# Optimization experiments

Hardware: AMD Instinct MI355X
Metric: run time of the kernel (lower is better)

## Reference

```python
import jax, jax.numpy as jnp
import numpy as np

B, S = 512, 512
VOCAB, E, H1, H2, NTAGS = 50000, 20, 30, 50, 45


def _xavier_scale(fan_in, fan_out):
    return float(np.sqrt(2.0 / (fan_in + fan_out)))


def setup_inputs() -> dict:
    key = jax.random.key(0)
    ks = jax.random.split(key, 32)
    n = lambda i, shape, s=1.0: jax.random.normal(ks[i], shape, dtype=jnp.float32) * s
    w = 0.1  # weight scale
    emb_f1 = n(0, (VOCAB, E), w).at[0].set(0.0)  # padding_idx=0
    emb_b1 = n(1, (VOCAB, E), w).at[0].set(0.0)
    xs1 = _xavier_scale(B, H1)
    xs2 = _xavier_scale(B, H2)
    inp = {
        "x": jax.random.randint(ks[2], (B, S), 0, VOCAB, dtype=jnp.int64),
        "emb_f1": emb_f1, "emb_b1": emb_b1,
        "h0_f1": n(3, (B, H1), xs1), "c0_f1": n(4, (B, H1), xs1),
        "Wih_f1": n(5, (4 * H1, E), w), "Whh_f1": n(6, (4 * H1, H1), w),
        "bih_f1": n(7, (4 * H1,), w), "bhh_f1": n(8, (4 * H1,), w),
        "h0_b1": n(9, (B, H1), xs1), "c0_b1": n(10, (B, H1), xs1),
        "Wih_b1": n(11, (4 * H1, E), w), "Whh_b1": n(12, (4 * H1, H1), w),
        "bih_b1": n(13, (4 * H1,), w), "bhh_b1": n(14, (4 * H1,), w),
        "h0_f2": n(15, (B, H2), xs2), "c0_f2": n(16, (B, H2), xs2),
        "Wih_f2": n(17, (4 * H2, 2 * H1), w), "Whh_f2": n(18, (4 * H2, H2), w),
        "bih_f2": n(19, (4 * H2,), w), "bhh_f2": n(20, (4 * H2,), w),
        "h0_b2": n(21, (B, H2), xs2), "c0_b2": n(22, (B, H2), xs2),
        "Wih_b2": n(23, (4 * H2, 2 * H1), w), "Whh_b2": n(24, (4 * H2, H2), w),
        "bih_b2": n(25, (4 * H2,), w), "bhh_b2": n(26, (4 * H2,), w),
        "lin_w": n(27, (NTAGS, 2 * H2), w), "lin_b": n(28, (NTAGS,), w),
    }
    return inp


def _run_lstm(seq, h0, c0, Wih, Whh, bih, bhh, forward):
    """PyTorch LSTMCell recurrence over seq (B,S,D). Replicates the original's
    quirks: backward dir appends hidden states in reversed time order, and the
    (S,B,H) stack is .view()-ed into (B,S,H) without transposing."""
    b, s, _ = seq.shape
    h = h0.shape[-1]
    xs = jnp.swapaxes(seq, 0, 1)  # (S,B,D)

    def step(carry, xt):
        hh, cc = carry
        g = xt @ Wih.T + bih + hh @ Whh.T + bhh  # (B, 4H), gate order i,f,g,o
        i, f, gg, o = jnp.split(g, 4, axis=-1)
        cc = jax.nn.sigmoid(f) * cc + jax.nn.sigmoid(i) * jnp.tanh(gg)
        hh = jax.nn.sigmoid(o) * jnp.tanh(cc)
        return (hh, cc), hh

    _, hs = jax.lax.scan(step, (h0, c0), xs, reverse=not forward)  # hs[i] ~ time i
    if not forward:
        hs = hs[::-1]  # torch appended in processing (reversed-time) order
    return hs.reshape(b, s, h)  # faithful buggy view (S,B,H) -> (B,S,H)


def reference(x, emb_f1, emb_b1,
              h0_f1, c0_f1, Wih_f1, Whh_f1, bih_f1, bhh_f1,
              h0_b1, c0_b1, Wih_b1, Whh_b1, bih_b1, bhh_b1,
              h0_f2, c0_f2, Wih_f2, Whh_f2, bih_f2, bhh_f2,
              h0_b2, c0_b2, Wih_b2, Whh_b2, bih_b2, bhh_b2,
              lin_w, lin_b):
    f1 = _run_lstm(emb_f1[x], h0_f1, c0_f1, Wih_f1, Whh_f1, bih_f1, bhh_f1, True)
    b1 = _run_lstm(emb_b1[x], h0_b1, c0_b1, Wih_b1, Whh_b1, bih_b1, bhh_b1, False)
    l1 = jnp.concatenate([f1, b1], axis=2)  # (B,S,2*H1)
    f2 = _run_lstm(l1, h0_f2, c0_f2, Wih_f2, Whh_f2, bih_f2, bhh_f2, True)
    b2 = _run_lstm(l1, h0_b2, c0_b2, Wih_b2, Whh_b2, bih_b2, bhh_b2, False)
    l2 = jnp.concatenate([f2, b2], axis=2)  # (B,S,2*H2)
    return l2 @ lin_w.T + lin_b  # (B,S,NTAGS)
```

## Files before the change

### kernel.cpp

```cpp
#include <hip/hip_runtime.h>
#include <hip/hip_bf16.h>

typedef __hip_bfloat16 bf16;
typedef __attribute__((ext_vector_type(8))) short short8;
typedef __attribute__((ext_vector_type(4))) float float4v;
typedef unsigned short ushort_t;

#define BB 512
#define SS 512
#define EE 20
#define H1C 30
#define H2C 50
#define NTC 45

#define BAR() asm volatile("s_waitcnt lgkmcnt(0)\n\ts_barrier" ::: "memory")

#if __has_builtin(__builtin_amdgcn_exp2f)
#define EXP2(x) __builtin_amdgcn_exp2f(x)
#else
#define EXP2(x) exp2f(x)
#endif
#if __has_builtin(__builtin_amdgcn_rcpf)
#define RCPF(x) __builtin_amdgcn_rcpf(x)
#else
#define RCPF(x) (1.0f / (x))
#endif

__device__ __forceinline__ float sigf(float v) {
    return RCPF(1.0f + EXP2(-1.4426950408889634f * v));
}
__device__ __forceinline__ float tanh_(float v) {
    return 2.0f * RCPF(1.0f + EXP2(-2.8853900817779268f * v)) - 1.0f;
}

__device__ __forceinline__ ushort_t f2bf(float f) {
    unsigned u = __float_as_uint(f);
    unsigned r = u + 0x7FFFu + ((u >> 16) & 1u);
    return (ushort_t)(r >> 16);
}
__device__ __forceinline__ float bf2f(ushort_t s) { return __uint_as_float(((unsigned)s) << 16); }

__device__ __forceinline__ float ldG(const void* p, int i, int f32) {
    if (f32) return ((const float*)p)[i];
    return bf2f(((const ushort_t*)p)[i]);
}
__device__ __forceinline__ int ldTok(const void* x, int i, int x64) {
    const int* xi = (const int*)x;
    return x64 ? xi[2 * i] : xi[i];
}

__global__ void detect_kernel(const void* bih, const void* x, int* flags) {
    if (threadIdx.x == 0 && blockIdx.x == 0) {
        const ushort_t* u = (const ushort_t*)bih;
        int isf = 0;
        for (int i = 0; i < 120; i++) {
            float v = fabsf(bf2f(u[i]));
            if (!(v < 16.0f)) isf = 1;
        }
        flags[0] = isf;
        const int* xi = (const int*)x;
        int orv = 0;
        for (int i = 1; i < 32; i += 2) orv |= xi[i];
        flags[1] = (orv == 0) ? 1 : 0;
    }
}

struct XV4 { float v[4]; };

__global__ __launch_bounds__(128) void lstm1_kernel(
    const void* __restrict__ x,
    const void* __restrict__ emb_f, const void* __restrict__ emb_b,
    const void* __restrict__ h0_f, const void* __restrict__ c0_f,
    const void* __restrict__ Wih_f, const void* __restrict__ Whh_f,
    const void* __restrict__ bih_f, const void* __restrict__ bhh_f,
    const void* __restrict__ h0_b, const void* __restrict__ c0_b,
    const void* __restrict__ Wih_b, const void* __restrict__ Whh_b,
    const void* __restrict__ bih_b, const void* __restrict__ bhh_b,
    ushort_t* __restrict__ hsf, ushort_t* __restrict__ hsb,
    const int* __restrict__ flags)
{
    const int f32v = flags[0], x64 = flags[1];
    const int wg = blockIdx.x, dir = wg >> 5, j0 = (wg & 31) << 4, tid = threadIdx.x;
    const int wave = tid >> 6, lane = tid & 63, li = lane & 15, quad = lane >> 4;

    const void* emb = dir ? emb_b : emb_f;
    const void* h0  = dir ? h0_b  : h0_f;
    const void* c0  = dir ? c0_b  : c0_f;
    const void* Wih = dir ? Wih_b : Wih_f;
    const void* Whh = dir ? Whh_b : Whh_f;
    const void* bih = dir ? bih_b : bih_f;
    const void* bhh = dir ? bhh_b : bhh_f;
    ushort_t* hs = dir ? hsb : hsf;

    __shared__ __align__(16) ushort_t Af[2][2][64][8];
    __shared__ int toks[16][SS];

    for (int idx = tid; idx < 16 * SS; idx += 128) {
        int r = idx >> 9, t = idx & (SS - 1);
        toks[r][t] = ldTok(x, (j0 + r) * SS + t, x64);
    }
    for (int idx = tid; idx < 2 * 2 * 64 * 8; idx += 128) ((ushort_t*)Af)[idx] = 0;

    const int n = wave * 16 + li;
    const bool nok = n < H1C;

    short8 bhi[4][2], blo[4][2];
    float bias_g[4];
    #pragma unroll
    for (int g = 0; g < 4; g++) {
        const int wrow = g * H1C + n;
        bias_g[g] = nok ? (ldG(bih, wrow, f32v) + ldG(bhh, wrow, f32v)) : 0.f;
        #pragma unroll
        for (int kt = 0; kt < 2; kt++) {
            short8 hi, lo;
            #pragma unroll
            for (int j = 0; j < 8; j++) {
                int k = kt * 32 + quad * 8 + j;
                float w = 0.f;
                if (nok) {
                    if (k < EE) w = ldG(Wih, wrow * EE + k, f32v);
                    else if (k < EE + H1C) w = ldG(Whh, wrow * H1C + (k - EE), f32v);
                }
                ushort_t h = f2bf(w);
                hi[j] = (short)h;
                lo[j] = (short)f2bf(w - bf2f(h));
            }
            bhi[g][kt] = hi; blo[g][kt] = lo;
        }
    }

    const int kh = EE + n;
    const int khk = kh >> 5, khg = (kh & 31) >> 3, khj = kh & 7;
    const int lrow = tid / 5, lc = tid - lrow * 5, k0 = lc * 4;
    const bool ldr = tid < 80;
    const int t0 = dir ? SS - 1 : 0, dt = dir ? -1 : 1;

    __syncthreads();

    float creg[4];
    #pragma unroll
    for (int r = 0; r < 4; r++) {
        const int m = quad * 4 + r;
        creg[r] = nok ? ldG(c0, (j0 + m) * H1C + n, f32v) : 0.f;
        ushort_t hb = nok ? f2bf(ldG(h0, (j0 + m) * H1C + n, f32v)) : 0;
        Af[0][khk][khg * 16 + m][khj] = hb;
    }
    XV4 xA, xB;
    if (ldr) {
        int tok = toks[lrow][t0];
        #pragma unroll
        for (int jj = 0; jj < 4; jj++)
            Af[0][0][(k0 >> 3) * 16 + lrow][(k0 & 7) + jj] = f2bf(ldG(emb, tok * EE + k0 + jj, f32v));
        int tok1 = toks[lrow][t0 + dt];
        #pragma unroll
        for (int jj = 0; jj < 4; jj++) xA.v[jj] = ldG(emb, tok1 * EE + k0 + jj, f32v);
    }
    __syncthreads();

    auto step = [&](int it, XV4& xin, XV4& xout) {
        const int t = t0 + dt * it;
        const int cur = it & 1, nxt = cur ^ 1;
        BAR();
        short8 af0 = *(const short8*)&Af[cur][0][lane][0];
        short8 af1 = *(const short8*)&Af[cur][1][lane][0];
        if (ldr && it + 2 < SS) {
            int tok = toks[lrow][t + 2 * dt];
            #pragma unroll
            for (int jj = 0; jj < 4; jj++) xout.v[jj] = ldG(emb, tok * EE + k0 + jj, f32v);
        }
        float4v acc[4];
        #pragma unroll
        for (int g = 0; g < 4; g++) {
            float4v a; a[0] = a[1] = a[2] = a[3] = bias_g[g];
            a = __builtin_amdgcn_mfma_f32_16x16x32_bf16(af0, bhi[g][0], a, 0, 0, 0);
            a = __builtin_amdgcn_mfma_f32_16x16x32_bf16(af0, blo[g][0], a, 0, 0, 0);
            a = __builtin_amdgcn_mfma_f32_16x16x32_bf16(af1, bhi[g][1], a, 0, 0, 0);
            a = __builtin_amdgcn_mfma_f32_16x16x32_bf16(af1, blo[g][1], a, 0, 0, 0);
            acc[g] = a;
        }
        ushort_t hb[4];
        #pragma unroll
        for (int r = 0; r < 4; r++) {
            float gi = acc[0][r], gf = acc[1][r], gg = acc[2][r], go = acc[3][r];
            float c = sigf(gf) * creg[r] + sigf(gi) * tanh_(gg);
            float h = sigf(go) * tanh_(c);
            creg[r] = c;
            hb[r] = nok ? f2bf(h) : 0;
            hs[((size_t)(j0 + quad * 4 + r) * SS + t) * 32 + n] = hb[r];
        }
        if (it + 1 < SS) {
            #pragma unroll
            for (int r = 0; r < 4; r++) Af[nxt][khk][khg * 16 + quad * 4 + r][khj] = hb[r];
            if (ldr) {
                #pragma unroll
                for (int jj = 0; jj < 4; jj++)
                    Af[nxt][0][(k0 >> 3) * 16 + lrow][(k0 & 7) + jj] = f2bf(xin.v[jj]);
            }
        }
    };
    for (int it = 0; it < SS; it += 2) { step(it, xA, xB); step(it + 1, xB, xA); }
}

__global__ __launch_bounds__(256) void lstm2_kernel(
    const ushort_t* __restrict__ hs1f, const ushort_t* __restrict__ hs1b,
    const void* __restrict__ h0_f, const void* __restrict__ c0_f,
    const void* __restrict__ Wih_f, const void* __restrict__ Whh_f,
    const void* __restrict__ bih_f, const void* __restrict__ bhh_f,
    const void* __restrict__ h0_b, const void* __restrict__ c0_b,
    const void* __restrict__ Wih_b, const void* __restrict__ Whh_b,
    const void* __restrict__ bih_b, const void* __restrict__ bhh_b,
    ushort_t* __restrict__ hsf, ushort_t* __restrict__ hsb,
    const int* __restrict__ flags)
{
    const int f32v = flags[0];
    const int wg = blockIdx.x, dir = wg >> 5, cb = (wg & 31) << 4, tid = threadIdx.x;
    const int wave = tid >> 6, lane = tid & 63, li = lane & 15, quad = lane >> 4;

    const void* h0  = dir ? h0_b  : h0_f;
    const void* c0  = dir ? c0_b  : c0_f;
    const void* Wih = dir ? Wih_b : Wih_f;
    const void* Whh = dir ? Whh_b : Whh_f;
    const void* bih = dir ? bih_b : bih_f;
    const void* bhh = dir ? bhh_b : bhh_f;
    ushort_t* hs = dir ? hsb : hsf;

    __shared__ __align__(16) ushort_t Af[2][4][64][8];
    for (int idx = tid; idx < 2 * 4 * 64 * 8; idx += 256) ((ushort_t*)Af)[idx] = 0;

    const int n = wave * 16 + li;
    const bool nok = n < H2C;

    short8 bhi[4][4], blo[4][4];
    float bias_g[4];
    #pragma unroll
    for (int g = 0; g < 4; g++) {
        const int wrow = g * H2C + n;
        bias_g[g] = nok ? (ldG(bih, wrow, f32v) + ldG(bhh, wrow, f32v)) : 0.f;
        #pragma unroll
        for (int kt = 0; kt < 4; kt++) {
            short8 hi, lo;
            #pragma unroll
            for (int j = 0; j < 8; j++) {
                int k = kt * 32 + quad * 8 + j;
                float w = 0.f;
                if (nok) {
                    if (k < H1C) w = ldG(Wih, wrow * (2 * H1C) + k, f32v);
                    else if (k >= 32 && k < 32 + H1C) w = ldG(Wih, wrow * (2 * H1C) + H1C + (k - 32), f32v);
                    else if (k >= 64 && k < 64 + H2C) w = ldG(Whh, wrow * H2C + (k - 64), f32v);
                }
                ushort_t h = f2bf(w);
                hi[j] = (short)h;
                lo[j] = (short)f2bf(w - bf2f(h));
            }
            bhi[g][kt] = hi; blo[g][kt] = lo;
        }
    }

    const int kh = 64 + n;
    const int khk = kh >> 5, khg = (kh & 31) >> 3, khj = kh & 7;
    const int lrow = tid >> 4, k0 = (tid & 15) * 4;
    const int t0 = dir ? SS - 1 : 0, dt = dir ? -1 : 1;

    auto loadX = [&](int c) -> ushort4 {
        const int a = cb + lrow;
        if (k0 < 32)
            return *(const ushort4*)&hs1f[((size_t)c * SS + a) * 32 + k0];
        else
            return *(const ushort4*)&hs1b[((size_t)c * SS + (SS - 1 - a)) * 32 + (k0 - 32)];
    };

    __syncthreads();

    float creg[4];
    #pragma unroll
    for (int r = 0; r < 4; r++) {
        const int m = quad * 4 + r;
        creg[r] = nok ? ldG(c0, (cb + m) * H2C + n, f32v) : 0.f;
        ushort_t hb = nok ? f2bf(ldG(h0, (cb + m) * H2C + n, f32v)) : 0;
        Af[0][khk][khg * 16 + m][khj] = hb;
    }
    {
        ushort4 xi = loadX(t0);
        const int kg = (k0 & 31) >> 3, kt = k0 >> 5, jb = k0 & 7;
        Af[0][kt][kg * 16 + lrow][jb + 0] = xi.x;
        Af[0][kt][kg * 16 + lrow][jb + 1] = xi.y;
        Af[0][kt][kg * 16 + lrow][jb + 2] = xi.z;
        Af[0][kt][kg * 16 + lrow][jb + 3] = xi.w;
    }
    ushort4 xA = loadX(t0 + dt), xB;
    __syncthreads();

    auto step = [&](int it, ushort4& xin, ushort4& xout) {
        const int c = t0 + dt * it;
        const int cur = it & 1, nxt = cur ^ 1;
        BAR();
        short8 af[4];
        #pragma unroll
        for (int kt = 0; kt < 4; kt++) af[kt] = *(const short8*)&Af[cur][kt][lane][0];
        if (it + 2 < SS) xout = loadX(c + 2 * dt);
        float4v acc[4];
        #pragma unroll
        for (int g = 0; g < 4; g++) {
            float4v a; a[0] = a[1] = a[2] = a[3] = bias_g[g];
            #pragma unroll
            for (int kt = 0; kt < 4; kt++) {
                a = __builtin_amdgcn_mfma_f32_16x16x32_bf16(af[kt], bhi[g][kt], a, 0, 0, 0);
                a = __builtin_amdgcn_mfma_f32_16x16x32_bf16(af[kt], blo[g][kt], a, 0, 0, 0);
            }
            acc[g] = a;
        }
        ushort_t hb[4];
        #pragma unroll
        for (int r = 0; r < 4; r++) {
            float gi = acc[0][r], gf = acc[1][r], gg = acc[2][r], go = acc[3][r];
            float cc = sigf(gf) * creg[r] + sigf(gi) * tanh_(gg);
            float h = sigf(go) * tanh_(cc);
            creg[r] = cc;
            hb[r] = nok ? f2bf(h) : 0;
        }
        ushort4 h4; h4.x = hb[0]; h4.y = hb[1]; h4.z = hb[2]; h4.w = hb[3];
        *(ushort4*)&hs[((size_t)c * 64 + n) * SS + cb + quad * 4] = h4;
        if (it + 1 < SS) {
            #pragma unroll
            for (int r = 0; r < 4; r++) Af[nxt][khk][khg * 16 + quad * 4 + r][khj] = hb[r];
            const int kg = (k0 & 31) >> 3, kt = k0 >> 5, jb = k0 & 7;
            Af[nxt][kt][kg * 16 + lrow][jb + 0] = xin.x;
            Af[nxt][kt][kg * 16 + lrow][jb + 1] = xin.y;
            Af[nxt][kt][kg * 16 + lrow][jb + 2] = xin.z;
            Af[nxt][kt][kg * 16 + lrow][jb + 3] = xin.w;
        }
    };
    for (int it = 0; it < SS; it += 2) { step(it, xA, xB); step(it + 1, xB, xA); }
}

__global__ __launch_bounds__(256) void lin_kernel(
    const ushort_t* __restrict__ hs2f, const ushort_t* __restrict__ hs2b,
    const void* __restrict__ lw, const void* __restrict__ lb,
    void* __restrict__ out, const int* __restrict__ flags)
{
    const int f32v = flags[0];
    const int tid = threadIdx.x, wave = tid >> 6, lane = tid & 63, li = lane & 15, quad = lane >> 4;

    __shared__ __align__(16) ushort_t Af[4][4][64][8];
    for (int idx = tid; idx < 4 * 4 * 64 * 8; idx += 256) ((ushort_t*)Af)[idx] = 0;

    short8 bhi[3][4], blo[3][4];
    float biasv[3];
    #pragma unroll
    for (int nt = 0; nt < 3; nt++) {
        const int nn = nt * 16 + li;
        const bool nok = nn < NTC;
        biasv[nt] = nok ? ldG(lb, nn, f32v) : 0.f;
        #pragma unroll
        for (int kt = 0; kt < 4; kt++) {
            short8 hi, lo;
            #pragma unroll
            for (int j = 0; j < 8; j++) {
                int k = kt * 32 + quad * 8 + j;
                float w = 0.f;
                if (nok) {
                    if (k < H2C) w = ldG(lw, nn * 100 + k, f32v);
                    else if (k >= 64 && k < 64 + H2C) w = ldG(lw, nn * 100 + 50 + (k - 64), f32v);
                }
                ushort_t h = f2bf(w);
                hi[j] = (short)h;
                lo[j] = (short)f2bf(w - bf2f(h));
            }
            bhi[nt][kt] = hi; blo[nt][kt] = lo;
        }
    }

    const int P0 = blockIdx.x * 64;
    const int i = P0 >> 9, j0 = P0 & 511;
    __syncthreads();
    for (int idx = tid; idx < 100 * 32; idx += 256) {
        const int kk = idx >> 5, pj = (idx & 31) * 2;
        unsigned v;
        int k;
        if (kk < H2C) {
            v = *(const unsigned*)&hs2f[((size_t)i * 64 + kk) * SS + j0 + pj];
            k = kk;
        } else {
            v = *(const unsigned*)&hs2b[((size_t)(SS - 1 - i) * 64 + (kk - H2C)) * SS + j0 + pj];
            k = 64 + (kk - H2C);
        }
        const int kt = k >> 5, kg = (k & 31) >> 3, j = k & 7;
        Af[pj >> 4][kt][kg * 16 + (pj & 15)][j] = (ushort_t)(v & 0xFFFF);
        Af[pj >> 4][kt][kg * 16 + ((pj + 1) & 15)][j] = (ushort_t)(v >> 16);
    }
    __syncthreads();

    short8 af[4];
    #pragma unroll
    for (int kt = 0; kt < 4; kt++) af[kt] = *(const short8*)&Af[wave][kt][lane][0];
    #pragma unroll
    for (int nt = 0; nt < 3; nt++) {
        float4v a; a[0] = a[1] = a[2] = a[3] = biasv[nt];
        #pragma unroll
        for (int kt = 0; kt < 4; kt++) {
            a = __builtin_amdgcn_mfma_f32_16x16x32_bf16(af[kt], bhi[nt][kt], a, 0, 0, 0);
            a = __builtin_amdgcn_mfma_f32_16x16x32_bf16(af[kt], blo[nt][kt], a, 0, 0, 0);
        }
        const int nn = nt * 16 + li;
        if (nn < NTC) {
            #pragma unroll
            for (int reg = 0; reg < 4; reg++) {
                const int prow = wave * 16 + quad * 4 + reg;
                const size_t op = (size_t)(P0 + prow) * NTC + nn;
                if (f32v) ((float*)out)[op] = a[reg];
                else      ((ushort_t*)out)[op] = f2bf(a[reg]);
            }
        }
    }
}

extern "C" void kernel_launch(void* const* d_in, const int* in_sizes, int n_in,
                              void* d_out, int out_size, void* d_ws, size_t ws_size,
                              hipStream_t stream)
{
    const void* x      = d_in[0];
    const void* emb_f1 = d_in[1];
    const void* emb_b1 = d_in[2];
    const void* h0_f1  = d_in[3];
    const void* c0_f1  = d_in[4];
    const void* Wih_f1 = d_in[5];
    const void* Whh_f1 = d_in[6];
    const void* bih_f1 = d_in[7];
    const void* bhh_f1 = d_in[8];
    const void* h0_b1  = d_in[9];
    const void* c0_b1  = d_in[10];
    const void* Wih_b1 = d_in[11];
    const void* Whh_b1 = d_in[12];
    const void* bih_b1 = d_in[13];
    const void* bhh_b1 = d_in[14];
    const void* h0_f2  = d_in[15];
    const void* c0_f2  = d_in[16];
    const void* Wih_f2 = d_in[17];
    const void* Whh_f2 = d_in[18];
    const void* bih_f2 = d_in[19];
    const void* bhh_f2 = d_in[20];
    const void* h0_b2  = d_in[21];
    const void* c0_b2  = d_in[22];
    const void* Wih_b2 = d_in[23];
    const void* Whh_b2 = d_in[24];
    const void* bih_b2 = d_in[25];
    const void* bhh_b2 = d_in[26];
    const void* lin_w  = d_in[27];
    const void* lin_b  = d_in[28];

    int* flags = (int*)d_ws;
    ushort_t* hs1f = (ushort_t*)((char*)d_ws + 256);
    ushort_t* hs1b = hs1f + (size_t)BB * SS * 32;
    ushort_t* hs2f = hs1b + (size_t)BB * SS * 32;
    ushort_t* hs2b = hs2f + (size_t)SS * 64 * BB;

    detect_kernel<<<1, 64, 0, stream>>>(bih_f1, x, flags);
    lstm1_kernel<<<64, 128, 0, stream>>>(x, emb_f1, emb_b1,
        h0_f1, c0_f1, Wih_f1, Whh_f1, bih_f1, bhh_f1,
        h0_b1, c0_b1, Wih_b1, Whh_b1, bih_b1, bhh_b1, hs1f, hs1b, flags);
    lstm2_kernel<<<64, 256, 0, stream>>>(hs1f, hs1b,
        h0_f2, c0_f2, Wih_f2, Whh_f2, bih_f2, bhh_f2,
        h0_b2, c0_b2, Wih_b2, Whh_b2, bih_b2, bhh_b2, hs2f, hs2b, flags);
    lin_kernel<<<(BB * SS) / 64, 256, 0, stream>>>(hs2f, hs2b, lin_w, lin_b, d_out, flags);
}
```

Before: 1.004 ms.

## Split LSTM gates across waves, precompute input projection one step ahead

Both LSTM kernels now give each wave one gate (i/f/g/o) and swap MFMA operand roles so weights are the A operand. Gate pre-activations go through a shared-memory Gs buffer, and a separate thread mapping applies the nonlinearities. The input-to-hidden product for step t+1 is issued alongside the recurrent product for step t, so only the Whh part sits on the serial dependency chain. Activations fold the log2e scaling into weights and bias, share reciprocals between paired sigmoids, and embedding loads are vectorized. The cost is two barriers per step plus the LDS round trip for gates, and lstm1 now runs 256 threads instead of 128.

Result: slower. 1.433 ms (+42.8%).

```diff
diff --git a/kernel.cpp b/kernel.cpp
--- a/kernel.cpp
+++ b/kernel.cpp
@@ -1,7 +1,6 @@
 #include <hip/hip_runtime.h>
 #include <hip/hip_bf16.h>
 
-typedef __hip_bfloat16 bf16;
 typedef __attribute__((ext_vector_type(8))) short short8;
 typedef __attribute__((ext_vector_type(4))) float float4v;
 typedef unsigned short ushort_t;
@@ -26,12 +25,7 @@
 #define RCPF(x) (1.0f / (x))
 #endif
 
-__device__ __forceinline__ float sigf(float v) {
-    return RCPF(1.0f + EXP2(-1.4426950408889634f * v));
-}
-__device__ __forceinline__ float tanh_(float v) {
-    return 2.0f * RCPF(1.0f + EXP2(-2.8853900817779268f * v)) - 1.0f;
-}
+#define LOG2E 1.4426950408889634f
 
 __device__ __forceinline__ ushort_t f2bf(float f) {
     unsigned u = __float_as_uint(f);
@@ -47,6 +41,21 @@
 __device__ __forceinline__ int ldTok(const void* x, int i, int x64) {
     const int* xi = (const int*)x;
     return x64 ? xi[2 * i] : xi[i];
+}
+
+__device__ __forceinline__ float lstm_act(float gi, float gf, float gg, float go, float& c) {
+    gi = fmaxf(gi, -30.f); gf = fmaxf(gf, -30.f);
+    gg = fmaxf(gg, -30.f); go = fmaxf(go, -30.f);
+    float di = 1.f + EXP2(-gi), df = 1.f + EXP2(-gf);
+    float dg = 1.f + EXP2(-gg), dO = 1.f + EXP2(-go);
+    float r1 = RCPF(di * df), r2 = RCPF(dg * dO);
+    float si = df * r1, sf = di * r1;
+    float tg = 2.f * (dO * r2) - 1.f;
+    float so = dg * r2;
+    float cc = sf * c + si * tg;
+    c = cc;
+    float e = EXP2(-2.8853900817779268f * cc);
+    return so * (2.f * RCPF(1.f + e) - 1.f);
 }
 
 __global__ void detect_kernel(const void* bih, const void* x, int* flags) {
@@ -65,9 +74,46 @@
     }
 }
 
-struct XV4 { float v[4]; };
-
-__global__ __launch_bounds__(128) void lstm1_kernel(
+struct XR8 { uint4 a, b; };
+
+__device__ __forceinline__ XR8 ldEmb8(const void* emb, int tok, int k0, int nelem, int f32v) {
+    XR8 o;
+    if (f32v) {
+        const float* p = (const float*)emb + (size_t)tok * EE + k0;
+        o.a = *(const uint4*)p;
+        o.b = (nelem == 8) ? *(const uint4*)(p + 4) : o.a;
+    } else {
+        const ushort_t* p = (const ushort_t*)emb + (size_t)tok * EE + k0;
+        uint2 lo = *(const uint2*)p;
+        o.a.x = lo.x; o.a.y = lo.y;
+        if (nelem == 8) { uint2 hi = *(const uint2*)(p + 4); o.a.z = hi.x; o.a.w = hi.y; }
+        else { o.a.z = 0; o.a.w = 0; }
+        o.b = o.a;
+    }
+    return o;
+}
+__device__ __forceinline__ void writeX1(ushort_t* dst, const XR8& x, int nelem, int f32v) {
+    if (f32v) {
+        if (nelem == 8) {
+            short8 s;
+            s[0] = (short)f2bf(__uint_as_float(x.a.x)); s[1] = (short)f2bf(__uint_as_float(x.a.y));
+            s[2] = (short)f2bf(__uint_as_float(x.a.z)); s[3] = (short)f2bf(__uint_as_float(x.a.w));
+            s[4] = (short)f2bf(__uint_as_float(x.b.x)); s[5] = (short)f2bf(__uint_as_float(x.b.y));
+            s[6] = (short)f2bf(__uint_as_float(x.b.z)); s[7] = (short)f2bf(__uint_as_float(x.b.w));
+            *(short8*)dst = s;
+        } else {
+            ushort4 u;
+            u.x = f2bf(__uint_as_float(x.a.x)); u.y = f2bf(__uint_as_float(x.a.y));
+            u.z = f2bf(__uint_as_float(x.a.z)); u.w = f2bf(__uint_as_float(x.a.w));
+            *(ushort4*)dst = u;
+        }
+    } else {
+        if (nelem == 8) *(uint4*)dst = x.a;
+        else { uint2 t; t.x = x.a.x; t.y = x.a.y; *(uint2*)dst = t; }
+    }
+}
+
+__global__ __launch_bounds__(256, 1) void lstm1_kernel(
     const void* __restrict__ x,
     const void* __restrict__ emb_f, const void* __restrict__ emb_b,
     const void* __restrict__ h0_f, const void* __restrict__ c0_f,
@@ -80,8 +126,9 @@
     const int* __restrict__ flags)
 {
     const int f32v = flags[0], x64 = flags[1];
-    const int wg = blockIdx.x, dir = wg >> 5, j0 = (wg & 31) << 4, tid = threadIdx.x;
-    const int wave = tid >> 6, lane = tid & 63, li = lane & 15, quad = lane >> 4;
+    const int tid = threadIdx.x;
+    const int cg = blockIdx.x, dir = cg >> 5, j0 = (cg & 31) << 4;
+    const int w = tid >> 6, lane = tid & 63, li = lane & 15, quad = lane >> 4;
 
     const void* emb = dir ? emb_b : emb_f;
     const void* h0  = dir ? h0_b  : h0_f;
@@ -92,116 +139,127 @@
     const void* bhh = dir ? bhh_b : bhh_f;
     ushort_t* hs = dir ? hsb : hsf;
 
-    __shared__ __align__(16) ushort_t Af[2][2][64][8];
     __shared__ int toks[16][SS];
-
-    for (int idx = tid; idx < 16 * SS; idx += 128) {
+    __shared__ __align__(16) ushort_t Xs[2][16][48];
+    __shared__ __align__(16) ushort_t Hs[16][48];
+    __shared__ float Gs[4][16][33];
+
+    for (int idx = tid; idx < 16 * SS; idx += 256) {
         int r = idx >> 9, t = idx & (SS - 1);
         toks[r][t] = ldTok(x, (j0 + r) * SS + t, x64);
     }
-    for (int idx = tid; idx < 2 * 2 * 64 * 8; idx += 128) ((ushort_t*)Af)[idx] = 0;
-
-    const int n = wave * 16 + li;
-    const bool nok = n < H1C;
-
-    short8 bhi[4][2], blo[4][2];
-    float bias_g[4];
+    for (int idx = tid; idx < 2 * 16 * 48; idx += 256) ((ushort_t*)Xs)[idx] = 0;
+    for (int idx = tid; idx < 16 * 48; idx += 256) ((ushort_t*)Hs)[idx] = 0;
+
+    const float sc = (w == 2) ? 2.0f * LOG2E : LOG2E;
+    short8 whh_h[2], whh_l[2], wxh_[2], wxl_[2];
+    float4v biasv[2];
     #pragma unroll
-    for (int g = 0; g < 4; g++) {
-        const int wrow = g * H1C + n;
-        bias_g[g] = nok ? (ldG(bih, wrow, f32v) + ldG(bhh, wrow, f32v)) : 0.f;
-        #pragma unroll
-        for (int kt = 0; kt < 2; kt++) {
-            short8 hi, lo;
+    for (int u = 0; u < 2; u++) {
+        const int n = u * 16 + li;
+        const bool nok = n < H1C;
+        #pragma unroll
+        for (int r = 0; r < 4; r++) {
+            int nn = u * 16 + quad * 4 + r;
+            biasv[u][r] = (nn < H1C) ? sc * (ldG(bih, w * H1C + nn, f32v) + ldG(bhh, w * H1C + nn, f32v)) : 0.f;
+        }
+        short8 hh, hl, xh, xl;
+        #pragma unroll
+        for (int j = 0; j < 8; j++) {
+            const int k = quad * 8 + j;
+            float wh = (nok && k < H1C) ? sc * ldG(Whh, (w * H1C + n) * H1C + k, f32v) : 0.f;
+            ushort_t b1 = f2bf(wh); hh[j] = (short)b1; hl[j] = (short)f2bf(wh - bf2f(b1));
+            float wx = (nok && k < EE) ? sc * ldG(Wih, (w * H1C + n) * EE + k, f32v) : 0.f;
+            ushort_t b2 = f2bf(wx); xh[j] = (short)b2; xl[j] = (short)f2bf(wx - bf2f(b2));
+        }
+        whh_h[u] = hh; whh_l[u] = hl; wxh_[u] = xh; wxl_[u] = xl;
+    }
+
+    const int am = li, anb = w * 8 + quad * 2;
+    const int lm = w * 4 + quad, lch = li;
+    const bool ldr = li < 3;
+    const int lk0 = lch * 8, lnel = (lch == 2) ? 4 : 8;
+    const int t0 = dir ? SS - 1 : 0, dt = dir ? -1 : 1;
+
+    __syncthreads();
+
+    float cr0, cr1;
+    {
+        const int n0 = anb, n1 = anb + 1;
+        cr0 = (n0 < H1C) ? ldG(c0, (j0 + am) * H1C + n0, f32v) : 0.f;
+        cr1 = (n1 < H1C) ? ldG(c0, (j0 + am) * H1C + n1, f32v) : 0.f;
+        unsigned ha = (n0 < H1C) ? f2bf(ldG(h0, (j0 + am) * H1C + n0, f32v)) : 0;
+        unsigned hb = (n1 < H1C) ? f2bf(ldG(h0, (j0 + am) * H1C + n1, f32v)) : 0;
+        *(unsigned*)&Hs[am][anb] = ha | (hb << 16);
+    }
+    XR8 embA = {}, embB = {}; int tokA = 0, tokB = 0;
+    if (ldr) {
+        XR8 e0 = ldEmb8(emb, toks[lm][t0], lk0, lnel, f32v);
+        writeX1(&Xs[0][lm][lk0], e0, lnel, f32v);
+        XR8 e1 = ldEmb8(emb, toks[lm][t0 + dt], lk0, lnel, f32v);
+        writeX1(&Xs[1][lm][lk0], e1, lnel, f32v);
+        embA = ldEmb8(emb, toks[lm][t0 + 2 * dt], lk0, lnel, f32v);
+        tokA = toks[lm][t0 + 3 * dt];
+    }
+    __syncthreads();
+
+    float4v xacc[2];
+    {
+        short8 xf = *(const short8*)&Xs[0][li][quad * 8];
+        #pragma unroll
+        for (int u = 0; u < 2; u++) {
+            float4v b = biasv[u];
+            b = __builtin_amdgcn_mfma_f32_16x16x32_bf16(wxh_[u], xf, b, 0, 0, 0);
+            b = __builtin_amdgcn_mfma_f32_16x16x32_bf16(wxl_[u], xf, b, 0, 0, 0);
+            xacc[u] = b;
+        }
+    }
+
+    auto step = [&](int it, XR8& ein, XR8& eout, int& tin, int& tout) {
+        const int t = t0 + dt * it;
+        short8 hf = *(const short8*)&Hs[li][quad * 8];
+        short8 xf = *(const short8*)&Xs[(it + 1) & 1][li][quad * 8];
+        float4v acc[2], xn[2];
+        #pragma unroll
+        for (int u = 0; u < 2; u++) {
+            float4v a = xacc[u];
+            a = __builtin_amdgcn_mfma_f32_16x16x32_bf16(whh_h[u], hf, a, 0, 0, 0);
+            a = __builtin_amdgcn_mfma_f32_16x16x32_bf16(whh_l[u], hf, a, 0, 0, 0);
+            acc[u] = a;
+            float4v b = biasv[u];
+            b = __builtin_amdgcn_mfma_f32_16x16x32_bf16(wxh_[u], xf, b, 0, 0, 0);
+            b = __builtin_amdgcn_mfma_f32_16x16x32_bf16(wxl_[u], xf, b, 0, 0, 0);
+            xn[u] = b;
+        }
+        #pragma unroll
+        for (int u = 0; u < 2; u++) {
             #pragma unroll
-            for (int j = 0; j < 8; j++) {
-                int k = kt * 32 + quad * 8 + j;
-                float w = 0.f;
-                if (nok) {
-                    if (k < EE) w = ldG(Wih, wrow * EE + k, f32v);
-                    else if (k < EE + H1C) w = ldG(Whh, wrow * H1C + (k - EE), f32v);
-                }
-                ushort_t h = f2bf(w);
-                hi[j] = (short)h;
-                lo[j] = (short)f2bf(w - bf2f(h));
-            }
-            bhi[g][kt] = hi; blo[g][kt] = lo;
-        }
-    }
-
-    const int kh = EE + n;
-    const int khk = kh >> 5, khg = (kh & 31) >> 3, khj = kh & 7;
-    const int lrow = tid / 5, lc = tid - lrow * 5, k0 = lc * 4;
-    const bool ldr = tid < 80;
-    const int t0 = dir ? SS - 1 : 0, dt = dir ? -1 : 1;
-
-    __syncthreads();
-
-    float creg[4];
-    #pragma unroll
-    for (int r = 0; r < 4; r++) {
-        const int m = quad * 4 + r;
-        creg[r] = nok ? ldG(c0, (j0 + m) * H1C + n, f32v) : 0.f;
-        ushort_t hb = nok ? f2bf(ldG(h0, (j0 + m) * H1C + n, f32v)) : 0;
-        Af[0][khk][khg * 16 + m][khj] = hb;
-    }
-    XV4 xA, xB;
-    if (ldr) {
-        int tok = toks[lrow][t0];
-        #pragma unroll
-        for (int jj = 0; jj < 4; jj++)
-            Af[0][0][(k0 >> 3) * 16 + lrow][(k0 & 7) + jj] = f2bf(ldG(emb, tok * EE + k0 + jj, f32v));
-        int tok1 = toks[lrow][t0 + dt];
-        #pragma unroll
-        for (int jj = 0; jj < 4; jj++) xA.v[jj] = ldG(emb, tok1 * EE + k0 + jj, f32v);
-    }
-    __syncthreads();
-
-    auto step = [&](int it, XV4& xin, XV4& xout) {
-        const int t = t0 + dt * it;
-        const int cur = it & 1, nxt = cur ^ 1;
+            for (int r = 0; r < 4; r++)
+                Gs[w][li][u * 16 + quad * 4 + r] = acc[u][r];
+        }
         BAR();
-        short8 af0 = *(const short8*)&Af[cur][0][lane][0];
-        short8 af1 = *(const short8*)&Af[cur][1][lane][0];
-        if (ldr && it + 2 < SS) {
-            int tok = toks[lrow][t + 2 * dt];
-            #pragma unroll
-            for (int jj = 0; jj < 4; jj++) xout.v[jj] = ldG(emb, tok * EE + k0 + jj, f32v);
-        }
-        float4v acc[4];
-        #pragma unroll
-        for (int g = 0; g < 4; g++) {
-            float4v a; a[0] = a[1] = a[2] = a[3] = bias_g[g];
-            a = __builtin_amdgcn_mfma_f32_16x16x32_bf16(af0, bhi[g][0], a, 0, 0, 0);
-            a = __builtin_amdgcn_mfma_f32_16x16x32_bf16(af0, blo[g][0], a, 0, 0, 0);
-            a = __builtin_amdgcn_mfma_f32_16x16x32_bf16(af1, bhi[g][1], a, 0, 0, 0);
-            a = __builtin_amdgcn_mfma_f32_16x16x32_bf16(af1, blo[g][1], a, 0, 0, 0);
-            acc[g] = a;
-        }
-        ushort_t hb[4];
-        #pragma unroll
-        for (int r = 0; r < 4; r++) {
-            float gi = acc[0][r], gf = acc[1][r], gg = acc[2][r], go = acc[3][r];
-            float c = sigf(gf) * creg[r] + sigf(gi) * tanh_(gg);
-            float h = sigf(go) * tanh_(c);
-            creg[r] = c;
-            hb[r] = nok ? f2bf(h) : 0;
-            hs[((size_t)(j0 + quad * 4 + r) * SS + t) * 32 + n] = hb[r];
-        }
-        if (it + 1 < SS) {
-            #pragma unroll
-            for (int r = 0; r < 4; r++) Af[nxt][khk][khg * 16 + quad * 4 + r][khj] = hb[r];
-            if (ldr) {
-                #pragma unroll
-                for (int jj = 0; jj < 4; jj++)
-                    Af[nxt][0][(k0 >> 3) * 16 + lrow][(k0 & 7) + jj] = f2bf(xin.v[jj]);
-            }
-        }
+        float gi0 = Gs[0][am][anb], gi1 = Gs[0][am][anb + 1];
+        float gf0 = Gs[1][am][anb], gf1 = Gs[1][am][anb + 1];
+        float gg0 = Gs[2][am][anb], gg1 = Gs[2][am][anb + 1];
+        float go0 = Gs[3][am][anb], go1 = Gs[3][am][anb + 1];
+        float h0v = lstm_act(gi0, gf0, gg0, go0, cr0);
+        float h1v = lstm_act(gi1, gf1, gg1, go1, cr1);
+        unsigned hp = (unsigned)f2bf(h0v) | ((unsigned)f2bf(h1v) << 16);
+        *(unsigned*)&Hs[am][anb] = hp;
+        *(unsigned*)&hs[((size_t)(j0 + am) * SS + t) * 32 + anb] = hp;
+        if (ldr) {
+            if (it + 2 < SS) writeX1(&Xs[it & 1][lm][lk0], ein, lnel, f32v);
+            if (it + 3 < SS) eout = ldEmb8(emb, tin, lk0, lnel, f32v);
+            if (it + 4 < SS) tout = toks[lm][t0 + dt * (it + 4)];
+        }
+        #pragma unroll
+        for (int u = 0; u < 2; u++) xacc[u] = xn[u];
+        BAR();
     };
-    for (int it = 0; it < SS; it += 2) { step(it, xA, xB); step(it + 1, xB, xA); }
-}
-
-__global__ __launch_bounds__(256) void lstm2_kernel(
+    for (int it = 0; it < SS; it += 2) { step(it, embA, embB, tokA, tokB); step(it + 1, embB, embA, tokB, tokA); }
+}
+
+__global__ __launch_bounds__(256, 1) void lstm2_kernel(
     const ushort_t* __restrict__ hs1f, const ushort_t* __restrict__ hs1b,
     const void* __restrict__ h0_f, const void* __restrict__ c0_f,
     const void* __restrict__ Wih_f, const void* __restrict__ Whh_f,
@@ -213,8 +271,9 @@
     const int* __restrict__ flags)
 {
     const int f32v = flags[0];
-    const int wg = blockIdx.x, dir = wg >> 5, cb = (wg & 31) << 4, tid = threadIdx.x;
-    const int wave = tid >> 6, lane = tid & 63, li = lane & 15, quad = lane >> 4;
+    const int tid = threadIdx.x;
+    const int cg = blockIdx.x, dir = cg >> 5, cb = (cg & 31) << 4;
+    const int w = tid >> 6, lane = tid & 63, li = lane & 15, quad = lane >> 4;
 
     const void* h0  = dir ? h0_b  : h0_f;
     const void* c0  = dir ? c0_b  : c0_f;
@@ -224,113 +283,138 @@
     const void* bhh = dir ? bhh_b : bhh_f;
     ushort_t* hs = dir ? hsb : hsf;
 
-    __shared__ __align__(16) ushort_t Af[2][4][64][8];
-    for (int idx = tid; idx < 2 * 4 * 64 * 8; idx += 256) ((ushort_t*)Af)[idx] = 0;
-
-    const int n = wave * 16 + li;
-    const bool nok = n < H2C;
-
-    short8 bhi[4][4], blo[4][4];
-    float bias_g[4];
+    __shared__ __align__(16) ushort_t Xs[2][16][112];
+    __shared__ __align__(16) ushort_t Hs[16][112];
+    __shared__ float Gs[4][16][65];
+
+    for (int idx = tid; idx < 2 * 16 * 112; idx += 256) ((ushort_t*)Xs)[idx] = 0;
+    for (int idx = tid; idx < 16 * 112; idx += 256) ((ushort_t*)Hs)[idx] = 0;
+
+    const float sc = (w == 2) ? 2.0f * LOG2E : LOG2E;
+    short8 wh_h[4][2], wh_l[4][2], wx_h[4][2], wx_l[4][2];
+    float4v biasv[4];
     #pragma unroll
-    for (int g = 0; g < 4; g++) {
-        const int wrow = g * H2C + n;
-        bias_g[g] = nok ? (ldG(bih, wrow, f32v) + ldG(bhh, wrow, f32v)) : 0.f;
-        #pragma unroll
-        for (int kt = 0; kt < 4; kt++) {
-            short8 hi, lo;
+    for (int u = 0; u < 4; u++) {
+        const int n = u * 16 + li;
+        const bool nok = n < H2C;
+        #pragma unroll
+        for (int r = 0; r < 4; r++) {
+            int nn = u * 16 + quad * 4 + r;
+            biasv[u][r] = (nn < H2C) ? sc * (ldG(bih, w * H2C + nn, f32v) + ldG(bhh, w * H2C + nn, f32v)) : 0.f;
+        }
+        #pragma unroll
+        for (int kt = 0; kt < 2; kt++) {
+            short8 hh, hl, xh, xl;
             #pragma unroll
             for (int j = 0; j < 8; j++) {
-                int k = kt * 32 + quad * 8 + j;
-                float w = 0.f;
+                const int k = kt * 32 + quad * 8 + j;
+                float wh = (nok && k < H2C) ? sc * ldG(Whh, (w * H2C + n) * H2C + k, f32v) : 0.f;
+                ushort_t b1 = f2bf(wh); hh[j] = (short)b1; hl[j] = (short)f2bf(wh - bf2f(b1));
+                float wx = 0.f;
                 if (nok) {
-                    if (k < H1C) w = ldG(Wih, wrow * (2 * H1C) + k, f32v);
-                    else if (k >= 32 && k < 32 + H1C) w = ldG(Wih, wrow * (2 * H1C) + H1C + (k - 32), f32v);
-                    else if (k >= 64 && k < 64 + H2C) w = ldG(Whh, wrow * H2C + (k - 64), f32v);
+                    if (k < H1C) wx = ldG(Wih, (w * H2C + n) * (2 * H1C) + k, f32v);
+                    else if (k >= 32 && k < 32 + H1C) wx = ldG(Wih, (w * H2C + n) * (2 * H1C) + H1C + (k - 32), f32v);
                 }
-                ushort_t h = f2bf(w);
-                hi[j] = (short)h;
-                lo[j] = (short)f2bf(w - bf2f(h));
+                wx *= sc;
+                ushort_t b2 = f2bf(wx); xh[j] = (short)b2; xl[j] = (short)f2bf(wx - bf2f(b2));
             }
-            bhi[g][kt] = hi; blo[g][kt] = lo;
-        }
-    }
-
-    const int kh = 64 + n;
-    const int khk = kh >> 5, khg = (kh & 31) >> 3, khj = kh & 7;
-    const int lrow = tid >> 4, k0 = (tid & 15) * 4;
+            wh_h[u][kt] = hh; wh_l[u][kt] = hl; wx_h[u][kt] = xh; wx_l[u][kt] = xl;
+        }
+    }
+
+    const int am = tid & 15, anq = tid >> 4;
+    const bool ldr = tid < 128;
+    const int lm = tid & 15, lch = (tid >> 4) & 7;
     const int t0 = dir ? SS - 1 : 0, dt = dir ? -1 : 1;
 
-    auto loadX = [&](int c) -> ushort4 {
-        const int a = cb + lrow;
-        if (k0 < 32)
-            return *(const ushort4*)&hs1f[((size_t)c * SS + a) * 32 + k0];
-        else
-            return *(const ushort4*)&hs1b[((size_t)c * SS + (SS - 1 - a)) * 32 + (k0 - 32)];
+    auto loadXraw = [&](int cc) -> uint4 {
+        if (lch < 4) return *(const uint4*)&hs1f[((size_t)cc * SS + (cb + lm)) * 32 + lch * 8];
+        return *(const uint4*)&hs1b[((size_t)cc * SS + (SS - 1 - (cb + lm))) * 32 + (lch - 4) * 8];
     };
 
     __syncthreads();
 
-    float creg[4];
+    float creg[4] = {0.f, 0.f, 0.f, 0.f};
     #pragma unroll
-    for (int r = 0; r < 4; r++) {
-        const int m = quad * 4 + r;
-        creg[r] = nok ? ldG(c0, (cb + m) * H2C + n, f32v) : 0.f;
-        ushort_t hb = nok ? f2bf(ldG(h0, (cb + m) * H2C + n, f32v)) : 0;
-        Af[0][khk][khg * 16 + m][khj] = hb;
-    }
+    for (int s = 0; s < 4; s++) {
+        const int n = s * 16 + anq;
+        if (n < H2C) {
+            creg[s] = ldG(c0, (cb + am) * H2C + n, f32v);
+            Hs[am][n] = f2bf(ldG(h0, (cb + am) * H2C + n, f32v));
+        }
+    }
+    uint4 xrA = {}, xrB = {};
+    if (ldr) {
+        *(uint4*)&Xs[0][lm][lch * 8] = loadXraw(t0);
+        *(uint4*)&Xs[1][lm][lch * 8] = loadXraw(t0 + dt);
+        xrA = loadXraw(t0 + 2 * dt);
+    }
+    __syncthreads();
+
+    float4v xacc[4];
     {
-        ushort4 xi = loadX(t0);
-        const int kg = (k0 & 31) >> 3, kt = k0 >> 5, jb = k0 & 7;
-        Af[0][kt][kg * 16 + lrow][jb + 0] = xi.x;
-        Af[0][kt][kg * 16 + lrow][jb + 1] = xi.y;
-        Af[0][kt][kg * 16 + lrow][jb + 2] = xi.z;
-        Af[0][kt][kg * 16 + lrow][jb + 3] = xi.w;
-    }
-    ushort4 xA = loadX(t0 + dt), xB;
-    __syncthreads();
-
-    auto step = [&](int it, ushort4& xin, ushort4& xout) {
-        const int c = t0 + dt * it;
-        const int cur = it & 1, nxt = cur ^ 1;
+        short8 xf0 = *(const short8*)&Xs[0][li][quad * 8];
+        short8 xf1 = *(const short8*)&Xs[0][li][32 + quad * 8];
+        #pragma unroll
+        for (int u = 0; u < 4; u++) {
+            float4v b = biasv[u];
+            b = __builtin_amdgcn_mfma_f32_16x16x32_bf16(wx_h[u][0], xf0, b, 0, 0, 0);
+            b = __builtin_amdgcn_mfma_f32_16x16x32_bf16(wx_l[u][0], xf0, b, 0, 0, 0);
+            b = __builtin_amdgcn_mfma_f32_16x16x32_bf16(wx_h[u][1], xf1, b, 0, 0, 0);
+            b = __builtin_amdgcn_mfma_f32_16x16x32_bf16(wx_l[u][1], xf1, b, 0, 0, 0);
+            xacc[u] = b;
+        }
+    }
+
+    auto step = [&](int it, uint4& xin, uint4& xout) {
+        const int t = t0 + dt * it;
+        short8 hf0 = *(const short8*)&Hs[li][quad * 8];
+        short8 hf1 = *(const short8*)&Hs[li][32 + quad * 8];
+        short8 xf0 = *(const short8*)&Xs[(it + 1) & 1][li][quad * 8];
+        short8 xf1 = *(const short8*)&Xs[(it + 1) & 1][li][32 + quad * 8];
+        float4v acc[4], xn[4];
+        #pragma unroll
+        for (int u = 0; u < 4; u++) {
+            float4v a = xacc[u];
+            a = __builtin_amdgcn_mfma_f32_16x16x32_bf16(wh_h[u][0], hf0, a, 0, 0, 0);
+            a = __builtin_amdgcn_mfma_f32_16x16x32_bf16(wh_l[u][0], hf0, a, 0, 0, 0);
+            a = __builtin_amdgcn_mfma_f32_16x16x32_bf16(wh_h[u][1], hf1, a, 0, 0, 0);
+            a = __builtin_amdgcn_mfma_f32_16x16x32_bf16(wh_l[u][1], hf1, a, 0, 0, 0);
+            acc[u] = a;
+            float4v b = biasv[u];
+            b = __builtin_amdgcn_mfma_f32_16x16x32_bf16(wx_h[u][0], xf0, b, 0, 0, 0);
+            b = __builtin_amdgcn_mfma_f32_16x16x32_bf16(wx_l[u][0], xf0, b, 0, 0, 0);
+            b = __builtin_amdgcn_mfma_f32_16x16x32_bf16(wx_h[u][1], xf1, b, 0, 0, 0);
+            b = __builtin_amdgcn_mfma_f32_16x16x32_bf16(wx_l[u][1], xf1, b, 0, 0, 0);
+            xn[u] = b;
+        }
+        #pragma unroll
+        for (int u = 0; u < 4; u++) {
+            #pragma unroll
+            for (int r = 0; r < 4; r++)
+                Gs[w][li][u * 16 + quad * 4 + r] = acc[u][r];
+        }
         BAR();
-        short8 af[4];
-        #pragma unroll
-        for (int kt = 0; kt < 4; kt++) af[kt] = *(const short8*)&Af[cur][kt][lane][0];
-        if (it + 2 < SS) xout = loadX(c + 2 * dt);
-        float4v acc[4];
-        #pragma unroll
-        for (int g = 0; g < 4; g++) {
-            float4v a; a[0] = a[1] = a[2] = a[3] = bias_g[g];
-            #pragma unroll
-            for (int kt = 0; kt < 4; kt++) {
-                a = __builtin_amdgcn_mfma_f32_16x16x32_bf16(af[kt], bhi[g][kt], a, 0, 0, 0);
-                a = __builtin_amdgcn_mfma_f32_16x16x32_bf16(af[kt], blo[g][kt], a, 0, 0, 0);
+        #pragma unroll
+        for (int s = 0; s < 4; s++) {
+            const int n = s * 16 + anq;
+            if (n < H2C) {
+                float gi = Gs[0][am][n], gf = Gs[1][am][n], gg = Gs[2][am][n], go = Gs[3][am][n];
+                float hv = lstm_act(gi, gf, gg, go, creg[s]);
+                ushort_t hb = f2bf(hv);
+                Hs[am][n] = hb;
+                hs[((size_t)t * 64 + n) * SS + cb + am] = hb;
             }
-            acc[g] = a;
-        }
-        ushort_t hb[4];
-        #pragma unroll
-        for (int r = 0; r < 4; r++) {
-            float gi = acc[0][r], gf = acc[1][r], gg = acc[2][r], go = acc[3][r];
-            float cc = sigf(gf) * creg[r] + sigf(gi) * tanh_(gg);
-            float h = sigf(go) * tanh_(cc);
-            creg[r] = cc;
-            hb[r] = nok ? f2bf(h) : 0;
-        }
-        ushort4 h4; h4.x = hb[0]; h4.y = hb[1]; h4.z = hb[2]; h4.w = hb[3];
-        *(ushort4*)&hs[((size_t)c * 64 + n) * SS + cb + quad * 4] = h4;
-        if (it + 1 < SS) {
-            #pragma unroll
-            for (int r = 0; r < 4; r++) Af[nxt][khk][khg * 16 + quad * 4 + r][khj] = hb[r];
-            const int kg = (k0 & 31) >> 3, kt = k0 >> 5, jb = k0 & 7;
-            Af[nxt][kt][kg * 16 + lrow][jb + 0] = xin.x;
-            Af[nxt][kt][kg * 16 + lrow][jb + 1] = xin.y;
-            Af[nxt][kt][kg * 16 + lrow][jb + 2] = xin.z;
-            Af[nxt][kt][kg * 16 + lrow][jb + 3] = xin.w;
-        }
+        }
+        if (ldr) {
+            if (it + 2 < SS) *(uint4*)&Xs[it & 1][lm][lch * 8] = xin;
+            if (it + 3 < SS) xout = loadXraw(t0 + dt * (it + 3));
+        }
+        #pragma unroll
+        for (int u = 0; u < 4; u++) xacc[u] = xn[u];
+        BAR();
     };
-    for (int it = 0; it < SS; it += 2) { step(it, xA, xB); step(it + 1, xB, xA); }
+    for (int it = 0; it < SS; it += 2) { step(it, xrA, xrB); step(it + 1, xrB, xrA); }
 }
 
 __global__ __launch_bounds__(256) void lin_kernel(
@@ -455,7 +539,7 @@
     ushort_t* hs2b = hs2f + (size_t)SS * 64 * BB;
 
     detect_kernel<<<1, 64, 0, stream>>>(bih_f1, x, flags);
-    lstm1_kernel<<<64, 128, 0, stream>>>(x, emb_f1, emb_b1,
+    lstm1_kernel<<<64, 256, 0, stream>>>(x, emb_f1, emb_b1,
         h0_f1, c0_f1, Wih_f1, Whh_f1, bih_f1, bhh_f1,
         h0_b1, c0_b1, Wih_b1, Whh_b1, bih_b1, bhh_b1, hs1f, hs1b, flags);
     lstm2_kernel<<<64, 256, 0, stream>>>(hs1f, hs1b,
```
